# Performance work log

Measured on AMD Instinct MI355X. Metric: run time of the kernel, lower is better.

## Reference

```python
import jax, jax.numpy as jnp
import numpy as np

B, N, D, H = 2, 2048, 512, 8
HD = D // H
EPS = 1e-5


def layernorm(x, g, b):
    m = jnp.mean(x, axis=-1, keepdims=True)
    v = jnp.var(x, axis=-1, keepdims=True)
    return (x - m) * jax.lax.rsqrt(v + EPS) * g + b


def setup_inputs() -> dict:
    key = jax.random.key(0)
    ks = jax.random.split(key, 16)
    s = 1.0 / np.sqrt(D)
    def lin(k, din, dout):
        k1, k2 = jax.random.split(k)
        return (jax.random.uniform(k1, (din, dout), jnp.float32, -s, s),
                jax.random.uniform(k2, (dout,), jnp.float32, -s, s))
    Wq, bq = lin(ks[0], D, D)
    Wk, bk = lin(ks[1], D, D)
    Wv, bv = lin(ks[2], D, D)
    Wo, bo = lin(ks[3], D, D)
    W1, b1 = lin(ks[4], D, 2 * D)
    W2, b2 = lin(ks[5], 2 * D, D)
    return {
        'y': jax.random.normal(ks[6], (B, N, D), jnp.float32),
        'Wq': Wq, 'bq': bq, 'Wk': Wk, 'bk': bk, 'Wv': Wv, 'bv': bv,
        'Wo': Wo, 'bo': bo,
        'ln1_g': jnp.ones((D,)), 'ln1_b': jnp.zeros((D,)),
        'ln2_g': jnp.ones((D,)), 'ln2_b': jnp.zeros((D,)),
        'W1': W1, 'b1': b1, 'W2': W2, 'b2': b2,
    }


def reference(y, Wq, bq, Wk, bk, Wv, bv, Wo, bo, ln1_g, ln1_b, ln2_g, ln2_b, W1, b1, W2, b2):
    x = layernorm(y, ln1_g, ln1_b)
    def heads(W, b):
        return (x @ W + b).reshape(B, N, H, HD).transpose(0, 2, 1, 3)  # bhnc
    q = heads(Wq, bq)
    k = heads(Wk, bk)
    v = heads(Wv, bv)
    score = jax.nn.softmax(jnp.einsum('bhic,bhjc->bhij', q, k) / np.sqrt(HD), axis=-1)
    r = jnp.einsum('bhij,bhjc->bhic', score, v)
    r = r.transpose(0, 2, 1, 3).reshape(B, N, D) @ Wo + bo
    y = y + r
    h = layernorm(y, ln2_g, ln2_b)
    h = jax.nn.gelu(h @ W1 + b1, approximate=False) @ W2 + b2
    return y + h
```

## Files before the change

### kernel.cpp

```cpp
#include <hip/hip_runtime.h>

#define DEVI __device__ __forceinline__

typedef unsigned short u16;
typedef unsigned int   u32;
typedef unsigned long long u64;
typedef float  f32x4  __attribute__((ext_vector_type(4)));
typedef __bf16 bf16x8 __attribute__((ext_vector_type(8)));

union FragU { bf16x8 b; u64 u[2]; __bf16 e[8]; };

DEVI u16 f2b(float x) { __bf16 t = (__bf16)x; return __builtin_bit_cast(u16, t); }

DEVI float exp2a(float x) { float r; asm("v_exp_f32 %0, %1" : "=v"(r) : "v"(x)); return r; }

DEVI void gload16(const void* g, void* l) {
  __builtin_amdgcn_global_load_lds((const __attribute__((address_space(1))) u32*)g,
                                   (__attribute__((address_space(3))) u32*)l, 16, 0, 0);
}

DEVI int swzo(int row, int kb) {
  return ((((kb >> 4) ^ row) & 7) << 4) | ((kb ^ row) & 8) | (kb & 7);
}

DEVI u64 ldswz(const char* base, int row, int kb) {
  return *reinterpret_cast<const u64*>(base + row * 128 + swzo(row, kb));
}

DEVI size_t gaddr(int row, int kbyte, int rowbytes) {
  return (size_t)row * rowbytes + (size_t)((kbyte & ~127) + swzo(row, kbyte & 127));
}

__global__ __launch_bounds__(256)
void transpose_all(const float* __restrict__ Wq, const float* __restrict__ Wk,
                   const float* __restrict__ Wv, const float* __restrict__ Wo,
                   const float* __restrict__ W1, const float* __restrict__ W2,
                   u16* __restrict__ wqkvT, u16* __restrict__ woT,
                   u16* __restrict__ w1T, u16* __restrict__ w2T) {
  __shared__ float tile[32][33];
  const int id = blockIdx.x;
  const float* src; u16* dst; int K, N, bx, by;
  if (id < 1024) {
    const int m = id >> 8, t = id & 255;
    K = 512; N = 512; bx = t & 15; by = t >> 4;
    src = (m == 0) ? Wq : (m == 1) ? Wk : (m == 2) ? Wv : Wo;
    dst = (m == 3) ? woT : wqkvT + m * 512 * 512;
  } else if (id < 1536) {
    const int t = id - 1024; K = 512; N = 1024; bx = t & 31; by = t >> 5;
    src = W1; dst = w1T;
  } else {
    const int t = id - 1536; K = 1024; N = 512; bx = t & 15; by = t >> 4;
    src = W2; dst = w2T;
  }
  const int tx = threadIdx.x & 31, ty = threadIdx.x >> 5;
#pragma unroll
  for (int i = 0; i < 4; ++i)
    tile[ty + i * 8][tx] = src[(size_t)(by * 32 + ty + i * 8) * N + bx * 32 + tx];
  __syncthreads();
#pragma unroll
  for (int i = 0; i < 4; ++i) {
    const int n = bx * 32 + ty + i * 8;
    const int k = by * 32 + tx;
    *(u16*)((char*)dst + gaddr(n, 2 * k, 2 * K)) = f2b(tile[tx][ty + i * 8]);
  }
}

__global__ __launch_bounds__(256)
void ln_bf16(const float* __restrict__ x, const float* __restrict__ g,
             const float* __restrict__ b, char* __restrict__ out) {
  const int row = blockIdx.x;
  const int t = threadIdx.x;
  const float2 v = ((const float2*)(x + (size_t)row * 512))[t];
  float s1 = v.x + v.y, s2 = v.x * v.x + v.y * v.y;
#pragma unroll
  for (int off = 32; off; off >>= 1) { s1 += __shfl_xor(s1, off); s2 += __shfl_xor(s2, off); }
  __shared__ float a1[4], a2[4];
  const int w = t >> 6;
  if ((t & 63) == 0) { a1[w] = s1; a2[w] = s2; }
  __syncthreads();
  s1 = a1[0] + a1[1] + a1[2] + a1[3];
  s2 = a2[0] + a2[1] + a2[2] + a2[3];
  const float mean = s1 * (1.f / 512.f);
  const float var = s2 * (1.f / 512.f) - mean * mean;
  const float rstd = rsqrtf(var + 1e-5f);
  const float2 gg = ((const float2*)g)[t];
  const float2 bb = ((const float2*)b)[t];
  const u16 o0 = f2b((v.x - mean) * rstd * gg.x + bb.x);
  const u16 o1 = f2b((v.y - mean) * rstd * gg.y + bb.y);
  *(u32*)(out + gaddr(row, 4 * t, 1024)) = (u32)o0 | ((u32)o1 << 16);
}

enum { EPI_QKV = 0, EPI_RES = 1, EPI_GELU = 2 };

template <int EPI, int WM, int WN, int AM, int AN>
__global__ __launch_bounds__(WM * WN * 64)
void gemm_bf16(const char* __restrict__ A, const char* __restrict__ Bt, int N, int K,
               const float* __restrict__ bias,
               const float* __restrict__ bq, const float* __restrict__ bk,
               const float* __restrict__ bv,
               const float* __restrict__ res, float* __restrict__ outF,
               char* __restrict__ outB,
               u16* __restrict__ qo, char* __restrict__ ko, char* __restrict__ vo) {
  constexpr int NW = WM * WN;
  constexpr int TM = WM * AM * 16, TN = WN * AN * 16;
  constexpr int NCHA = TM / 8, NCHB = TN / 8, NCH = NCHA + NCHB;
  constexpr int CPW = NCH / NW;
  static_assert(CPW * NW == NCH, "chunk split");
  __shared__ __align__(16) char sA[2][TM * 128];
  __shared__ __align__(16) char sB[2][TN * 128];
  const int tid = threadIdx.x;
  const int l = tid & 63, w = tid >> 6;
  const int tm = blockIdx.x, tn = blockIdx.y;
  const int wr = w / WN, wc = w % WN;
  const int u = l >> 4, r16 = l & 15;
  const int lrow = l >> 3, lgr = l & 7;
  f32x4 acc[AM][AN] = {};
  const size_t KB = (size_t)K * 2;
  const char* Ab = A + (size_t)(tm * TM) * KB;
  const char* Bb = Bt + (size_t)(tn * TN) * KB;
  const int nkt = K >> 6;
  auto stage = [&](int buf, int kt) {
#pragma unroll
    for (int i = 0; i < CPW; ++i) {
      const int c = w * CPW + i;
      if (c < NCHA) {
        gload16(Ab + (size_t)(c * 8 + lrow) * KB + (size_t)kt * 128 + (lgr << 4),
                sA[buf] + c * 1024);
      } else {
        const int c2 = c - NCHA;
        gload16(Bb + (size_t)(c2 * 8 + lrow) * KB + (size_t)kt * 128 + (lgr << 4),
                sB[buf] + c2 * 1024);
      }
    }
  };
  stage(0, 0);
  int cur = 0;
  for (int kt = 0; kt < nkt; ++kt) {
    __syncthreads();
    if (kt + 1 < nkt) stage(cur ^ 1, kt + 1);
    __builtin_amdgcn_s_setprio(1);
#pragma unroll
    for (int ks = 0; ks < 2; ++ks) {
      FragU af[AM], bfr[AN];
      const int kb = ks * 64 + (u << 3);
#pragma unroll
      for (int i = 0; i < AM; ++i) {
        af[i].u[0] = ldswz(sA[cur], wr * (AM * 16) + i * 16 + r16, kb);
        af[i].u[1] = ldswz(sA[cur], wr * (AM * 16) + i * 16 + r16, kb + 32);
      }
#pragma unroll
      for (int i = 0; i < AN; ++i) {
        bfr[i].u[0] = ldswz(sB[cur], wc * (AN * 16) + i * 16 + r16, kb);
        bfr[i].u[1] = ldswz(sB[cur], wc * (AN * 16) + i * 16 + r16, kb + 32);
      }
#pragma unroll
      for (int mi = 0; mi < AM; ++mi)
#pragma unroll
        for (int ni = 0; ni < AN; ++ni)
          acc[mi][ni] = __builtin_amdgcn_mfma_f32_16x16x32_bf16(af[mi].b, bfr[ni].b,
                                                                acc[mi][ni], 0, 0, 0);
    }
    __builtin_amdgcn_s_setprio(0);
    cur ^= 1;
  }
  const int row0 = tm * TM + wr * (AM * 16) + (u << 2);
  const int col0 = tn * TN + wc * (AN * 16) + r16;
#pragma unroll
  for (int mi = 0; mi < AM; ++mi) {
#pragma unroll
    for (int ni = 0; ni < AN; ++ni) {
      const int col = col0 + ni * 16;
      if (EPI == EPI_RES) {
#pragma unroll
        for (int r = 0; r < 4; ++r) {
          const int row = row0 + mi * 16 + r;
          outF[(size_t)row * N + col] = acc[mi][ni][r] + bias[col] + res[(size_t)row * N + col];
        }
      } else if (EPI == EPI_GELU) {
#pragma unroll
        for (int r = 0; r < 4; ++r) {
          const int row = row0 + mi * 16 + r;
          const float x = acc[mi][ni][r] + bias[col];
          *(u16*)(outB + gaddr(row, 2 * col, 2 * N)) =
              f2b(0.5f * x * (1.f + erff(x * 0.70710678118f)));
        }
      } else {
        const int which = col >> 9, cc = col & 511;
        const int h = cc >> 6, hd = cc & 63;
        if (which == 2) {
          const int rowa = row0 + mi * 16;
          const int bb2 = rowa >> 11, nt0 = rowa & 2047;
          const int bh = bb2 * 8 + h;
          const float bvv = bv[cc];
          union { ushort4 s; u64 q; } pk;
          pk.s.x = f2b(acc[mi][ni][0] + bvv);
          pk.s.y = f2b(acc[mi][ni][1] + bvv);
          pk.s.z = f2b(acc[mi][ni][2] + bvv);
          pk.s.w = f2b(acc[mi][ni][3] + bvv);
          *(u64*)(vo + (size_t)bh * 262144 + (size_t)(nt0 >> 6) * 8192 +
                  gaddr(hd, 2 * (nt0 & 63), 128)) = pk.q;
        } else {
#pragma unroll
          for (int r = 0; r < 4; ++r) {
            const int row = row0 + mi * 16 + r;
            const int bb2 = row >> 11, nt = row & 2047;
            const int bh = bb2 * 8 + h;
            if (which == 0)
              qo[((size_t)bh * 2048 + nt) * 64 + hd] = f2b((acc[mi][ni][r] + bq[cc]) * 0.18033688f);
            else
              *(u16*)(ko + (size_t)bh * 262144 + (size_t)(nt >> 6) * 8192 +
                      gaddr(nt & 63, 2 * hd, 128)) = f2b(acc[mi][ni][r] + bk[cc]);
          }
        }
      }
    }
  }
}

__global__ __launch_bounds__(512)
void attn_k(const u16* __restrict__ q, const char* __restrict__ kswz,
            const char* __restrict__ vswz, char* __restrict__ r_out) {
  __shared__ __align__(16) char sK[2][2][8192];
  __shared__ __align__(16) char sV[2][2][8192];
  const int tid = threadIdx.x;
  const int l = tid & 63, w = tid >> 6;
  const int kvh = w & 1, qw = w >> 1;
  const int bh = blockIdx.x, qt = blockIdx.y;
  const int u = l >> 4, r16 = l & 15;
  const char* kp = kswz + (size_t)bh * 262144;
  const char* vp = vswz + (size_t)bh * 262144;
  const int c0 = qw * 2;
  auto stage = [&](int buf, int t) {
#pragma unroll
    for (int c = 0; c < 2; ++c) {
      gload16(kp + (size_t)t * 8192 + (c0 + c) * 1024 + l * 16, sK[kvh][buf] + (c0 + c) * 1024);
      gload16(vp + (size_t)t * 8192 + (c0 + c) * 1024 + l * 16, sV[kvh][buf] + (c0 + c) * 1024);
    }
  };
  stage(0, kvh * 16);
  FragU qf[2];
  {
    const u16* qr = q + (size_t)bh * (2048 * 64) + (size_t)(qt * 64 + qw * 16 + r16) * 64 + (u << 2);
    qf[0].u[0] = *(const u64*)qr;        qf[0].u[1] = *(const u64*)(qr + 16);
    qf[1].u[0] = *(const u64*)(qr + 32); qf[1].u[1] = *(const u64*)(qr + 48);
  }
  float mrun = -1e30f, lrun = 0.f;
  f32x4 o[4] = {};
  int cur = 0;
  for (int i = 0; i < 16; ++i) {
    __syncthreads();
    if (i < 15) stage(cur ^ 1, kvh * 16 + i + 1);
    f32x4 st[4] = {};
    __builtin_amdgcn_s_setprio(1);
#pragma unroll
    for (int ks = 0; ks < 2; ++ks) {
      const int kb = ks * 64 + (u << 3);
#pragma unroll
      for (int mi = 0; mi < 4; ++mi) {
        FragU kf;
        kf.u[0] = ldswz(sK[kvh][cur], mi * 16 + r16, kb);
        kf.u[1] = ldswz(sK[kvh][cur], mi * 16 + r16, kb + 32);
        st[mi] = __builtin_amdgcn_mfma_f32_16x16x32_bf16(kf.b, qf[ks].b, st[mi], 0, 0, 0);
      }
    }
    __builtin_amdgcn_s_setprio(0);
    float tmax = -1e30f;
#pragma unroll
    for (int mi = 0; mi < 4; ++mi)
#pragma unroll
      for (int r = 0; r < 4; ++r) tmax = fmaxf(tmax, st[mi][r]);
    tmax = fmaxf(tmax, __shfl_xor(tmax, 16));
    tmax = fmaxf(tmax, __shfl_xor(tmax, 32));
    if (!__all(tmax <= mrun + 11.5f)) {
      const float mnew = fmaxf(mrun, tmax);
      const float alpha = exp2a(mrun - mnew);
      lrun *= alpha;
#pragma unroll
      for (int mo = 0; mo < 4; ++mo) o[mo] *= alpha;
      mrun = mnew;
    }
    float p[4][4];
    float tsum = 0.f;
#pragma unroll
    for (int mi = 0; mi < 4; ++mi)
#pragma unroll
      for (int r = 0; r < 4; ++r) { p[mi][r] = exp2a(st[mi][r] - mrun); tsum += p[mi][r]; }
    tsum += __shfl_xor(tsum, 16);
    tsum += __shfl_xor(tsum, 32);
    lrun += tsum;
    FragU pb[2];
#pragma unroll
    for (int ks = 0; ks < 2; ++ks)
#pragma unroll
      for (int j = 0; j < 4; ++j) {
        pb[ks].e[j]     = (__bf16)p[2 * ks][j];
        pb[ks].e[j + 4] = (__bf16)p[2 * ks + 1][j];
      }
    __builtin_amdgcn_s_setprio(1);
#pragma unroll
    for (int ks = 0; ks < 2; ++ks) {
      const int kb = ks * 64 + (u << 3);
#pragma unroll
      for (int mo = 0; mo < 4; ++mo) {
        FragU vf;
        vf.u[0] = ldswz(sV[kvh][cur], mo * 16 + r16, kb);
        vf.u[1] = ldswz(sV[kvh][cur], mo * 16 + r16, kb + 32);
        o[mo] = __builtin_amdgcn_mfma_f32_16x16x32_bf16(vf.b, pb[ks].b, o[mo], 0, 0, 0);
      }
    }
    __builtin_amdgcn_s_setprio(0);
    cur ^= 1;
  }
  __syncthreads();
  float* scrO  = (float*)&sK[0][0][0];
  float* scrML = (float*)&sV[0][0][0];
  if (kvh == 1) {
    if (u == 0) { scrML[qw * 32 + r16] = mrun; scrML[qw * 32 + 16 + r16] = lrun; }
#pragma unroll
    for (int mo = 0; mo < 4; ++mo)
#pragma unroll
      for (int r = 0; r < 4; ++r)
        scrO[qw * 1024 + (mo * 16 + u * 4 + r) * 16 + r16] = o[mo][r];
  }
  __syncthreads();
  if (kvh == 0) {
    const float m1 = scrML[qw * 32 + r16], l1 = scrML[qw * 32 + 16 + r16];
    const float m = fmaxf(mrun, m1);
    const float a0 = exp2a(mrun - m), a1 = exp2a(m1 - m);
    const float linv = 1.f / (lrun * a0 + l1 * a1);
    const float f0 = a0 * linv, f1 = a1 * linv;
    const int tok = (bh >> 3) * 2048 + qt * 64 + qw * 16 + r16;
    const int h = bh & 7;
#pragma unroll
    for (int mo = 0; mo < 4; ++mo) {
      union { ushort4 s; u64 qq; } pk;
      float vv[4];
#pragma unroll
      for (int r = 0; r < 4; ++r)
        vv[r] = o[mo][r] * f0 + scrO[qw * 1024 + (mo * 16 + u * 4 + r) * 16 + r16] * f1;
      pk.s.x = f2b(vv[0]); pk.s.y = f2b(vv[1]); pk.s.z = f2b(vv[2]); pk.s.w = f2b(vv[3]);
      *(u64*)(r_out + (size_t)tok * 1024 + h * 128 + swzo(tok, mo * 32 + (u << 3))) = pk.qq;
    }
  }
}

extern "C" void kernel_launch(void* const* d_in, const int* in_sizes, int n_in,
                              void* d_out, int out_size, void* d_ws, size_t ws_size,
                              hipStream_t stream) {
  const float* y    = (const float*)d_in[0];
  const float* Wq   = (const float*)d_in[1];
  const float* bq   = (const float*)d_in[2];
  const float* Wk   = (const float*)d_in[3];
  const float* bk   = (const float*)d_in[4];
  const float* Wv   = (const float*)d_in[5];
  const float* bv   = (const float*)d_in[6];
  const float* Wo   = (const float*)d_in[7];
  const float* bo   = (const float*)d_in[8];
  const float* ln1g = (const float*)d_in[9];
  const float* ln1b = (const float*)d_in[10];
  const float* ln2g = (const float*)d_in[11];
  const float* ln2b = (const float*)d_in[12];
  const float* W1   = (const float*)d_in[13];
  const float* b1   = (const float*)d_in[14];
  const float* W2   = (const float*)d_in[15];
  const float* b2   = (const float*)d_in[16];
  float* out = (float*)d_out;
  char* ws = (char*)d_ws;
  char* xb    = ws;
  u16*  qb    = (u16*)(ws + (4u << 20));
  char* kswz  = ws + (8u << 20);
  char* vswz  = ws + (12u << 20);
  char* rb    = ws + (16u << 20);
  char* g1b   = ws + (20u << 20);
  u16* wqkvT  = (u16*)(ws + (28u << 20));
  u16* woT    = wqkvT + 1536 * 512;
  u16* w1T    = woT + 512 * 512;
  u16* w2T    = w1T + 1024 * 512;

  transpose_all<<<2048, 256, 0, stream>>>(Wq, Wk, Wv, Wo, W1, W2, wqkvT, woT, w1T, w2T);
  ln_bf16<<<4096, 256, 0, stream>>>(y, ln1g, ln1b, xb);
  gemm_bf16<EPI_QKV, 2, 2, 4, 2><<<dim3(32, 24), 256, 0, stream>>>(
      xb, (const char*)wqkvT, 1536, 512, nullptr, bq, bk, bv,
      nullptr, nullptr, nullptr, qb, kswz, vswz);
  attn_k<<<dim3(16, 32), 512, 0, stream>>>(qb, kswz, vswz, rb);
  gemm_bf16<EPI_RES, 2, 2, 2, 2><<<dim3(64, 8), 256, 0, stream>>>(
      rb, (const char*)woT, 512, 512, bo, nullptr, nullptr, nullptr,
      y, out, nullptr, nullptr, nullptr, nullptr);
  ln_bf16<<<4096, 256, 0, stream>>>(out, ln2g, ln2b, xb);
  gemm_bf16<EPI_GELU, 2, 2, 4, 2><<<dim3(32, 16), 256, 0, stream>>>(
      xb, (const char*)w1T, 1024, 512, b1, nullptr, nullptr, nullptr,
      nullptr, nullptr, g1b, nullptr, nullptr, nullptr);
  gemm_bf16<EPI_RES, 2, 2, 2, 2><<<dim3(64, 8), 256, 0, stream>>>(
      g1b, (const char*)w2T, 512, 1024, b2, nullptr, nullptr, nullptr,
      out, out, nullptr, nullptr, nullptr, nullptr);
}
```

Baseline: 104.8 us.

## Fuse weight transpose with first layernorm and fuse Wo GEMM with second layernorm

Merges the weight-transpose kernel and the first layernorm into one launch with branch on block index. Replaces the Wo projection GEMM plus separate layernorm with a new kernel where each 512-thread block computes a full 16-row by 512-column output tile, adds bias and residual, reduces row statistics across waves, and writes both the fp32 residual stream and the bf16 normalized activations. This removes two launches and a round trip of the residual through memory, at the cost of only 256 blocks with B fragments loaded directly from global memory per wave.

```diff
diff --git a/kernel.cpp b/kernel.cpp
--- a/kernel.cpp
+++ b/kernel.cpp
@@ -32,62 +32,62 @@
 }
 
 __global__ __launch_bounds__(256)
-void transpose_all(const float* __restrict__ Wq, const float* __restrict__ Wk,
-                   const float* __restrict__ Wv, const float* __restrict__ Wo,
-                   const float* __restrict__ W1, const float* __restrict__ W2,
-                   u16* __restrict__ wqkvT, u16* __restrict__ woT,
-                   u16* __restrict__ w1T, u16* __restrict__ w2T) {
-  __shared__ float tile[32][33];
+void prep(const float* __restrict__ Wq, const float* __restrict__ Wk,
+          const float* __restrict__ Wv, const float* __restrict__ Wo,
+          const float* __restrict__ W1, const float* __restrict__ W2,
+          u16* __restrict__ wqkvT, u16* __restrict__ woT,
+          u16* __restrict__ w1T, u16* __restrict__ w2T,
+          const float* __restrict__ y, const float* __restrict__ ln1g,
+          const float* __restrict__ ln1b, char* __restrict__ xb) {
   const int id = blockIdx.x;
-  const float* src; u16* dst; int K, N, bx, by;
-  if (id < 1024) {
-    const int m = id >> 8, t = id & 255;
-    K = 512; N = 512; bx = t & 15; by = t >> 4;
-    src = (m == 0) ? Wq : (m == 1) ? Wk : (m == 2) ? Wv : Wo;
-    dst = (m == 3) ? woT : wqkvT + m * 512 * 512;
-  } else if (id < 1536) {
-    const int t = id - 1024; K = 512; N = 1024; bx = t & 31; by = t >> 5;
-    src = W1; dst = w1T;
+  if (id < 2048) {
+    __shared__ float tile[32][33];
+    const float* src; u16* dst; int K, N, bx, by;
+    if (id < 1024) {
+      const int m = id >> 8, t = id & 255;
+      K = 512; N = 512; bx = t & 15; by = t >> 4;
+      src = (m == 0) ? Wq : (m == 1) ? Wk : (m == 2) ? Wv : Wo;
+      dst = (m == 3) ? woT : wqkvT + m * 512 * 512;
+    } else if (id < 1536) {
+      const int t = id - 1024; K = 512; N = 1024; bx = t & 31; by = t >> 5;
+      src = W1; dst = w1T;
+    } else {
+      const int t = id - 1536; K = 1024; N = 512; bx = t & 15; by = t >> 4;
+      src = W2; dst = w2T;
+    }
+    const int tx = threadIdx.x & 31, ty = threadIdx.x >> 5;
+#pragma unroll
+    for (int i = 0; i < 4; ++i)
+      tile[ty + i * 8][tx] = src[(size_t)(by * 32 + ty + i * 8) * N + bx * 32 + tx];
+    __syncthreads();
+#pragma unroll
+    for (int i = 0; i < 4; ++i) {
+      const int n = bx * 32 + ty + i * 8;
+      const int k = by * 32 + tx;
+      *(u16*)((char*)dst + gaddr(n, 2 * k, 2 * K)) = f2b(tile[tx][ty + i * 8]);
+    }
   } else {
-    const int t = id - 1536; K = 1024; N = 512; bx = t & 15; by = t >> 4;
-    src = W2; dst = w2T;
-  }
-  const int tx = threadIdx.x & 31, ty = threadIdx.x >> 5;
-#pragma unroll
-  for (int i = 0; i < 4; ++i)
-    tile[ty + i * 8][tx] = src[(size_t)(by * 32 + ty + i * 8) * N + bx * 32 + tx];
-  __syncthreads();
-#pragma unroll
-  for (int i = 0; i < 4; ++i) {
-    const int n = bx * 32 + ty + i * 8;
-    const int k = by * 32 + tx;
-    *(u16*)((char*)dst + gaddr(n, 2 * k, 2 * K)) = f2b(tile[tx][ty + i * 8]);
-  }
-}
-
-__global__ __launch_bounds__(256)
-void ln_bf16(const float* __restrict__ x, const float* __restrict__ g,
-             const float* __restrict__ b, char* __restrict__ out) {
-  const int row = blockIdx.x;
-  const int t = threadIdx.x;
-  const float2 v = ((const float2*)(x + (size_t)row * 512))[t];
-  float s1 = v.x + v.y, s2 = v.x * v.x + v.y * v.y;
-#pragma unroll
-  for (int off = 32; off; off >>= 1) { s1 += __shfl_xor(s1, off); s2 += __shfl_xor(s2, off); }
-  __shared__ float a1[4], a2[4];
-  const int w = t >> 6;
-  if ((t & 63) == 0) { a1[w] = s1; a2[w] = s2; }
-  __syncthreads();
-  s1 = a1[0] + a1[1] + a1[2] + a1[3];
-  s2 = a2[0] + a2[1] + a2[2] + a2[3];
-  const float mean = s1 * (1.f / 512.f);
-  const float var = s2 * (1.f / 512.f) - mean * mean;
-  const float rstd = rsqrtf(var + 1e-5f);
-  const float2 gg = ((const float2*)g)[t];
-  const float2 bb = ((const float2*)b)[t];
-  const u16 o0 = f2b((v.x - mean) * rstd * gg.x + bb.x);
-  const u16 o1 = f2b((v.y - mean) * rstd * gg.y + bb.y);
-  *(u32*)(out + gaddr(row, 4 * t, 1024)) = (u32)o0 | ((u32)o1 << 16);
+    const int row = id - 2048;
+    const int t = threadIdx.x;
+    const float2 v = ((const float2*)(y + (size_t)row * 512))[t];
+    float s1 = v.x + v.y, s2 = v.x * v.x + v.y * v.y;
+#pragma unroll
+    for (int off = 32; off; off >>= 1) { s1 += __shfl_xor(s1, off); s2 += __shfl_xor(s2, off); }
+    __shared__ float a1[4], a2[4];
+    const int w = t >> 6;
+    if ((t & 63) == 0) { a1[w] = s1; a2[w] = s2; }
+    __syncthreads();
+    s1 = a1[0] + a1[1] + a1[2] + a1[3];
+    s2 = a2[0] + a2[1] + a2[2] + a2[3];
+    const float mean = s1 * (1.f / 512.f);
+    const float var = s2 * (1.f / 512.f) - mean * mean;
+    const float rstd = rsqrtf(var + 1e-5f);
+    const float2 gg = ((const float2*)ln1g)[t];
+    const float2 bb = ((const float2*)ln1b)[t];
+    const u16 o0 = f2b((v.x - mean) * rstd * gg.x + bb.x);
+    const u16 o1 = f2b((v.y - mean) * rstd * gg.y + bb.y);
+    *(u32*)(xb + gaddr(row, 4 * t, 1024)) = (u32)o0 | ((u32)o1 << 16);
+  }
 }
 
 enum { EPI_QKV = 0, EPI_RES = 1, EPI_GELU = 2 };
@@ -213,6 +213,125 @@
           }
         }
       }
+    }
+  }
+}
+
+__global__ __launch_bounds__(512)
+void gemm_res_ln(const char* __restrict__ A, const char* __restrict__ Bt,
+                 const float* __restrict__ bo, const float* __restrict__ yres,
+                 float* __restrict__ outF, const float* __restrict__ g2,
+                 const float* __restrict__ b2v, char* __restrict__ xout) {
+  __shared__ __align__(16) char sA[2][2048];
+  __shared__ float red[2][8][16];
+  __shared__ float stats[2][16];
+  const int tid = threadIdx.x;
+  const int l = tid & 63, w = tid >> 6;
+  const int tm = blockIdx.x;
+  const int u = l >> 4, r16 = l & 15;
+  const int lrow = l >> 3, lgr = l & 7;
+  const char* Ab = A + (size_t)(tm * 16) * 1024;
+  f32x4 acc[4] = {};
+  FragU pa[8], pb[8];
+  auto loadB = [&](FragU* ps, int kt) {
+#pragma unroll
+    for (int ks = 0; ks < 2; ++ks) {
+      const int kb = ks * 64 + (u << 3);
+#pragma unroll
+      for (int ni = 0; ni < 4; ++ni) {
+        const int col = w * 64 + ni * 16 + r16;
+        const char* bp = Bt + (size_t)col * 1024 + kt * 128;
+        ps[ks * 4 + ni].u[0] = *(const u64*)(bp + swzo(col, kb));
+        ps[ks * 4 + ni].u[1] = *(const u64*)(bp + swzo(col, kb + 32));
+      }
+    }
+  };
+  auto stageA = [&](int buf, int kt) {
+    if (w < 2)
+      gload16(Ab + (size_t)(w * 8 + lrow) * 1024 + (size_t)kt * 128 + (lgr << 4),
+              sA[buf] + w * 1024);
+  };
+  auto mmaStep = [&](FragU* ps, int buf) {
+#pragma unroll
+    for (int ks = 0; ks < 2; ++ks) {
+      const int kb = ks * 64 + (u << 3);
+      FragU af;
+      af.u[0] = ldswz(sA[buf], r16, kb);
+      af.u[1] = ldswz(sA[buf], r16, kb + 32);
+#pragma unroll
+      for (int ni = 0; ni < 4; ++ni)
+        acc[ni] = __builtin_amdgcn_mfma_f32_16x16x32_bf16(af.b, ps[ks * 4 + ni].b,
+                                                          acc[ni], 0, 0, 0);
+    }
+  };
+  stageA(0, 0);
+  loadB(pa, 0);
+#pragma unroll
+  for (int kt2 = 0; kt2 < 4; ++kt2) {
+    const int kt = kt2 * 2;
+    __syncthreads();
+    stageA(1, kt + 1);
+    loadB(pb, kt + 1);
+    __builtin_amdgcn_s_setprio(1);
+    mmaStep(pa, 0);
+    __builtin_amdgcn_s_setprio(0);
+    __syncthreads();
+    if (kt + 2 < 8) { stageA(0, kt + 2); loadB(pa, kt + 2); }
+    __builtin_amdgcn_s_setprio(1);
+    mmaStep(pb, 1);
+    __builtin_amdgcn_s_setprio(0);
+  }
+  float x[4][4];
+  float s1r[4] = {}, s2r[4] = {};
+#pragma unroll
+  for (int ni = 0; ni < 4; ++ni) {
+    const int col = w * 64 + ni * 16 + r16;
+#pragma unroll
+    for (int rr = 0; rr < 4; ++rr) {
+      const int row = tm * 16 + u * 4 + rr;
+      const float v = acc[ni][rr] + bo[col] + yres[(size_t)row * 512 + col];
+      x[ni][rr] = v;
+      s1r[rr] += v;
+      s2r[rr] += v * v;
+    }
+  }
+#pragma unroll
+  for (int off = 1; off < 16; off <<= 1) {
+#pragma unroll
+    for (int rr = 0; rr < 4; ++rr) {
+      s1r[rr] += __shfl_xor(s1r[rr], off);
+      s2r[rr] += __shfl_xor(s2r[rr], off);
+    }
+  }
+  if (r16 == 0) {
+#pragma unroll
+    for (int rr = 0; rr < 4; ++rr) {
+      red[0][w][u * 4 + rr] = s1r[rr];
+      red[1][w][u * 4 + rr] = s2r[rr];
+    }
+  }
+  __syncthreads();
+  if (tid < 16) {
+    float s1 = 0.f, s2 = 0.f;
+#pragma unroll
+    for (int ww = 0; ww < 8; ++ww) { s1 += red[0][ww][tid]; s2 += red[1][ww][tid]; }
+    const float mean = s1 * (1.f / 512.f);
+    const float var = s2 * (1.f / 512.f) - mean * mean;
+    stats[0][tid] = mean;
+    stats[1][tid] = rsqrtf(var + 1e-5f);
+  }
+  __syncthreads();
+#pragma unroll
+  for (int ni = 0; ni < 4; ++ni) {
+    const int col = w * 64 + ni * 16 + r16;
+    const float gg = g2[col], bb = b2v[col];
+#pragma unroll
+    for (int rr = 0; rr < 4; ++rr) {
+      const int rl = u * 4 + rr;
+      const int row = tm * 16 + rl;
+      outF[(size_t)row * 512 + col] = x[ni][rr];
+      const float ln = (x[ni][rr] - stats[0][rl]) * stats[1][rl] * gg + bb;
+      *(u16*)(xout + gaddr(row, 2 * col, 1024)) = f2b(ln);
     }
   }
 }
@@ -377,16 +496,14 @@
   u16* w1T    = woT + 512 * 512;
   u16* w2T    = w1T + 1024 * 512;
 
-  transpose_all<<<2048, 256, 0, stream>>>(Wq, Wk, Wv, Wo, W1, W2, wqkvT, woT, w1T, w2T);
-  ln_bf16<<<4096, 256, 0, stream>>>(y, ln1g, ln1b, xb);
+  prep<<<6144, 256, 0, stream>>>(Wq, Wk, Wv, Wo, W1, W2, wqkvT, woT, w1T, w2T,
+                                 y, ln1g, ln1b, xb);
   gemm_bf16<EPI_QKV, 2, 2, 4, 2><<<dim3(32, 24), 256, 0, stream>>>(
       xb, (const char*)wqkvT, 1536, 512, nullptr, bq, bk, bv,
       nullptr, nullptr, nullptr, qb, kswz, vswz);
   attn_k<<<dim3(16, 32), 512, 0, stream>>>(qb, kswz, vswz, rb);
-  gemm_bf16<EPI_RES, 2, 2, 2, 2><<<dim3(64, 8), 256, 0, stream>>>(
-      rb, (const char*)woT, 512, 512, bo, nullptr, nullptr, nullptr,
-      y, out, nullptr, nullptr, nullptr, nullptr);
-  ln_bf16<<<4096, 256, 0, stream>>>(out, ln2g, ln2b, xb);
+  gemm_res_ln<<<256, 512, 0, stream>>>(
+      rb, (const char*)woT, bo, y, out, ln2g, ln2b, xb);
   gemm_bf16<EPI_GELU, 2, 2, 4, 2><<<dim3(32, 16), 256, 0, stream>>>(
       xb, (const char*)w1T, 1024, 512, b1, nullptr, nullptr, nullptr,
       nullptr, nullptr, g1b, nullptr, nullptr, nullptr);
```

Result: no change. 106.4 us (+1.5%).

## Merge weight transpose with first layernorm; restructure attention K/V staging

Applied to the files above, without the earlier changes.

The weight transpose and the first layernorm now run as a single launch, which removes one kernel launch and its tail. The transpose also writes packed 8-byte stores instead of 2-byte scalar stores. The attention kernel now processes two KV tiles per iteration, with K and V loaded into both buffers and restaged separately. The next K block loads while softmax and PV run, and the next V block loads after PV. This halves the loop trips and barriers but raises register pressure (8 score accumulators) and drops the old double-buffered overlap of QK with loads.

```diff
diff --git a/kernel.cpp b/kernel.cpp
--- a/kernel.cpp
+++ b/kernel.cpp
@@ -32,36 +32,64 @@
 }
 
 __global__ __launch_bounds__(256)
-void transpose_all(const float* __restrict__ Wq, const float* __restrict__ Wk,
-                   const float* __restrict__ Wv, const float* __restrict__ Wo,
-                   const float* __restrict__ W1, const float* __restrict__ W2,
-                   u16* __restrict__ wqkvT, u16* __restrict__ woT,
-                   u16* __restrict__ w1T, u16* __restrict__ w2T) {
-  __shared__ float tile[32][33];
+void prep(const float* __restrict__ Wq, const float* __restrict__ Wk,
+          const float* __restrict__ Wv, const float* __restrict__ Wo,
+          const float* __restrict__ W1, const float* __restrict__ W2,
+          u16* __restrict__ wqkvT, u16* __restrict__ woT,
+          u16* __restrict__ w1T, u16* __restrict__ w2T,
+          const float* __restrict__ y, const float* __restrict__ ln1g,
+          const float* __restrict__ ln1b, char* __restrict__ xb) {
   const int id = blockIdx.x;
-  const float* src; u16* dst; int K, N, bx, by;
-  if (id < 1024) {
-    const int m = id >> 8, t = id & 255;
-    K = 512; N = 512; bx = t & 15; by = t >> 4;
-    src = (m == 0) ? Wq : (m == 1) ? Wk : (m == 2) ? Wv : Wo;
-    dst = (m == 3) ? woT : wqkvT + m * 512 * 512;
-  } else if (id < 1536) {
-    const int t = id - 1024; K = 512; N = 1024; bx = t & 31; by = t >> 5;
-    src = W1; dst = w1T;
+  if (id < 2048) {
+    __shared__ float tile[32][33];
+    const float* src; u16* dst; int K, N, bx, by;
+    if (id < 1024) {
+      const int m = id >> 8, t = id & 255;
+      K = 512; N = 512; bx = t & 15; by = t >> 4;
+      src = (m == 0) ? Wq : (m == 1) ? Wk : (m == 2) ? Wv : Wo;
+      dst = (m == 3) ? woT : wqkvT + m * 512 * 512;
+    } else if (id < 1536) {
+      const int t = id - 1024; K = 512; N = 1024; bx = t & 31; by = t >> 5;
+      src = W1; dst = w1T;
+    } else {
+      const int t = id - 1536; K = 1024; N = 512; bx = t & 15; by = t >> 4;
+      src = W2; dst = w2T;
+    }
+    const int tx = threadIdx.x & 31, ty = threadIdx.x >> 5;
+#pragma unroll
+    for (int i = 0; i < 4; ++i)
+      tile[ty + i * 8][tx] = src[(size_t)(by * 32 + ty + i * 8) * N + bx * 32 + tx];
+    __syncthreads();
+    const int nl = threadIdx.x >> 3, kq = threadIdx.x & 7;
+    const int n = bx * 32 + nl;
+    const int kg = by * 32 + kq * 4;
+    union { ushort4 s; u64 q; } pk;
+    pk.s.x = f2b(tile[kq * 4 + 0][nl]);
+    pk.s.y = f2b(tile[kq * 4 + 1][nl]);
+    pk.s.z = f2b(tile[kq * 4 + 2][nl]);
+    pk.s.w = f2b(tile[kq * 4 + 3][nl]);
+    *(u64*)((char*)dst + gaddr(n, 2 * kg, 2 * K)) = pk.q;
   } else {
-    const int t = id - 1536; K = 1024; N = 512; bx = t & 15; by = t >> 4;
-    src = W2; dst = w2T;
-  }
-  const int tx = threadIdx.x & 31, ty = threadIdx.x >> 5;
-#pragma unroll
-  for (int i = 0; i < 4; ++i)
-    tile[ty + i * 8][tx] = src[(size_t)(by * 32 + ty + i * 8) * N + bx * 32 + tx];
-  __syncthreads();
-#pragma unroll
-  for (int i = 0; i < 4; ++i) {
-    const int n = bx * 32 + ty + i * 8;
-    const int k = by * 32 + tx;
-    *(u16*)((char*)dst + gaddr(n, 2 * k, 2 * K)) = f2b(tile[tx][ty + i * 8]);
+    const int row = id - 2048;
+    const int t = threadIdx.x;
+    const float2 v = ((const float2*)(y + (size_t)row * 512))[t];
+    float s1 = v.x + v.y, s2 = v.x * v.x + v.y * v.y;
+#pragma unroll
+    for (int off = 32; off; off >>= 1) { s1 += __shfl_xor(s1, off); s2 += __shfl_xor(s2, off); }
+    __shared__ float a1[4], a2[4];
+    const int w = t >> 6;
+    if ((t & 63) == 0) { a1[w] = s1; a2[w] = s2; }
+    __syncthreads();
+    s1 = a1[0] + a1[1] + a1[2] + a1[3];
+    s2 = a2[0] + a2[1] + a2[2] + a2[3];
+    const float mean = s1 * (1.f / 512.f);
+    const float var = s2 * (1.f / 512.f) - mean * mean;
+    const float rstd = rsqrtf(var + 1e-5f);
+    const float2 gg = ((const float2*)ln1g)[t];
+    const float2 bb = ((const float2*)ln1b)[t];
+    const u16 o0 = f2b((v.x - mean) * rstd * gg.x + bb.x);
+    const u16 o1 = f2b((v.y - mean) * rstd * gg.y + bb.y);
+    *(u32*)(xb + gaddr(row, 4 * t, 1024)) = (u32)o0 | ((u32)o1 << 16);
   }
 }
 
@@ -230,14 +258,24 @@
   const char* kp = kswz + (size_t)bh * 262144;
   const char* vp = vswz + (size_t)bh * 262144;
   const int c0 = qw * 2;
-  auto stage = [&](int buf, int t) {
+  auto stageK = [&](int j) {
+    const size_t t0 = (size_t)(kvh * 16 + 2 * j) * 8192;
 #pragma unroll
     for (int c = 0; c < 2; ++c) {
-      gload16(kp + (size_t)t * 8192 + (c0 + c) * 1024 + l * 16, sK[kvh][buf] + (c0 + c) * 1024);
-      gload16(vp + (size_t)t * 8192 + (c0 + c) * 1024 + l * 16, sV[kvh][buf] + (c0 + c) * 1024);
+      gload16(kp + t0 + (c0 + c) * 1024 + l * 16, sK[kvh][0] + (c0 + c) * 1024);
+      gload16(kp + t0 + 8192 + (c0 + c) * 1024 + l * 16, sK[kvh][1] + (c0 + c) * 1024);
     }
   };
-  stage(0, kvh * 16);
+  auto stageV = [&](int j) {
+    const size_t t0 = (size_t)(kvh * 16 + 2 * j) * 8192;
+#pragma unroll
+    for (int c = 0; c < 2; ++c) {
+      gload16(vp + t0 + (c0 + c) * 1024 + l * 16, sV[kvh][0] + (c0 + c) * 1024);
+      gload16(vp + t0 + 8192 + (c0 + c) * 1024 + l * 16, sV[kvh][1] + (c0 + c) * 1024);
+    }
+  };
+  stageK(0);
+  stageV(0);
   FragU qf[2];
   {
     const u16* qr = q + (size_t)bh * (2048 * 64) + (size_t)(qt * 64 + qw * 16 + r16) * 64 + (u << 2);
@@ -246,29 +284,32 @@
   }
   float mrun = -1e30f, lrun = 0.f;
   f32x4 o[4] = {};
-  int cur = 0;
-  for (int i = 0; i < 16; ++i) {
+  __syncthreads();
+  for (int j = 0; j < 8; ++j) {
+    f32x4 st[8] = {};
+    __builtin_amdgcn_s_setprio(1);
+#pragma unroll
+    for (int buf = 0; buf < 2; ++buf)
+#pragma unroll
+      for (int ks = 0; ks < 2; ++ks) {
+        const int kb = ks * 64 + (u << 3);
+#pragma unroll
+        for (int mi = 0; mi < 4; ++mi) {
+          FragU kf;
+          kf.u[0] = ldswz(sK[kvh][buf], mi * 16 + r16, kb);
+          kf.u[1] = ldswz(sK[kvh][buf], mi * 16 + r16, kb + 32);
+          st[buf * 4 + mi] = __builtin_amdgcn_mfma_f32_16x16x32_bf16(kf.b, qf[ks].b,
+                                                                     st[buf * 4 + mi], 0, 0, 0);
+        }
+      }
+    __builtin_amdgcn_s_setprio(0);
     __syncthreads();
-    if (i < 15) stage(cur ^ 1, kvh * 16 + i + 1);
-    f32x4 st[4] = {};
-    __builtin_amdgcn_s_setprio(1);
-#pragma unroll
-    for (int ks = 0; ks < 2; ++ks) {
-      const int kb = ks * 64 + (u << 3);
-#pragma unroll
-      for (int mi = 0; mi < 4; ++mi) {
-        FragU kf;
-        kf.u[0] = ldswz(sK[kvh][cur], mi * 16 + r16, kb);
-        kf.u[1] = ldswz(sK[kvh][cur], mi * 16 + r16, kb + 32);
-        st[mi] = __builtin_amdgcn_mfma_f32_16x16x32_bf16(kf.b, qf[ks].b, st[mi], 0, 0, 0);
-      }
-    }
-    __builtin_amdgcn_s_setprio(0);
+    if (j < 7) stageK(j + 1);
     float tmax = -1e30f;
 #pragma unroll
-    for (int mi = 0; mi < 4; ++mi)
-#pragma unroll
-      for (int r = 0; r < 4; ++r) tmax = fmaxf(tmax, st[mi][r]);
+    for (int i = 0; i < 8; ++i)
+#pragma unroll
+      for (int r = 0; r < 4; ++r) tmax = fmaxf(tmax, st[i][r]);
     tmax = fmaxf(tmax, __shfl_xor(tmax, 16));
     tmax = fmaxf(tmax, __shfl_xor(tmax, 32));
     if (!__all(tmax <= mrun + 11.5f)) {
@@ -279,37 +320,42 @@
       for (int mo = 0; mo < 4; ++mo) o[mo] *= alpha;
       mrun = mnew;
     }
-    float p[4][4];
     float tsum = 0.f;
 #pragma unroll
-    for (int mi = 0; mi < 4; ++mi)
-#pragma unroll
-      for (int r = 0; r < 4; ++r) { p[mi][r] = exp2a(st[mi][r] - mrun); tsum += p[mi][r]; }
+    for (int i = 0; i < 8; ++i)
+#pragma unroll
+      for (int r = 0; r < 4; ++r) { st[i][r] = exp2a(st[i][r] - mrun); tsum += st[i][r]; }
     tsum += __shfl_xor(tsum, 16);
     tsum += __shfl_xor(tsum, 32);
     lrun += tsum;
-    FragU pb[2];
-#pragma unroll
-    for (int ks = 0; ks < 2; ++ks)
-#pragma unroll
-      for (int j = 0; j < 4; ++j) {
-        pb[ks].e[j]     = (__bf16)p[2 * ks][j];
-        pb[ks].e[j + 4] = (__bf16)p[2 * ks + 1][j];
-      }
+    FragU pb[4];
+#pragma unroll
+    for (int buf = 0; buf < 2; ++buf)
+#pragma unroll
+      for (int ks = 0; ks < 2; ++ks)
+#pragma unroll
+        for (int jj = 0; jj < 4; ++jj) {
+          pb[buf * 2 + ks].e[jj]     = (__bf16)st[buf * 4 + 2 * ks][jj];
+          pb[buf * 2 + ks].e[jj + 4] = (__bf16)st[buf * 4 + 2 * ks + 1][jj];
+        }
     __builtin_amdgcn_s_setprio(1);
 #pragma unroll
-    for (int ks = 0; ks < 2; ++ks) {
-      const int kb = ks * 64 + (u << 3);
-#pragma unroll
-      for (int mo = 0; mo < 4; ++mo) {
-        FragU vf;
-        vf.u[0] = ldswz(sV[kvh][cur], mo * 16 + r16, kb);
-        vf.u[1] = ldswz(sV[kvh][cur], mo * 16 + r16, kb + 32);
-        o[mo] = __builtin_amdgcn_mfma_f32_16x16x32_bf16(vf.b, pb[ks].b, o[mo], 0, 0, 0);
-      }
-    }
+    for (int buf = 0; buf < 2; ++buf)
+#pragma unroll
+      for (int ks = 0; ks < 2; ++ks) {
+        const int kb = ks * 64 + (u << 3);
+#pragma unroll
+        for (int mo = 0; mo < 4; ++mo) {
+          FragU vf;
+          vf.u[0] = ldswz(sV[kvh][buf], mo * 16 + r16, kb);
+          vf.u[1] = ldswz(sV[kvh][buf], mo * 16 + r16, kb + 32);
+          o[mo] = __builtin_amdgcn_mfma_f32_16x16x32_bf16(vf.b, pb[buf * 2 + ks].b,
+                                                          o[mo], 0, 0, 0);
+        }
+      }
     __builtin_amdgcn_s_setprio(0);
-    cur ^= 1;
+    __syncthreads();
+    if (j < 7) stageV(j + 1);
   }
   __syncthreads();
   float* scrO  = (float*)&sK[0][0][0];
@@ -377,8 +423,8 @@
   u16* w1T    = woT + 512 * 512;
   u16* w2T    = w1T + 1024 * 512;
 
-  transpose_all<<<2048, 256, 0, stream>>>(Wq, Wk, Wv, Wo, W1, W2, wqkvT, woT, w1T, w2T);
-  ln_bf16<<<4096, 256, 0, stream>>>(y, ln1g, ln1b, xb);
+  prep<<<6144, 256, 0, stream>>>(Wq, Wk, Wv, Wo, W1, W2, wqkvT, woT, w1T, w2T,
+                                 y, ln1g, ln1b, xb);
   gemm_bf16<EPI_QKV, 2, 2, 4, 2><<<dim3(32, 24), 256, 0, stream>>>(
       xb, (const char*)wqkvT, 1536, 512, nullptr, bq, bk, bv,
       nullptr, nullptr, nullptr, qb, kswz, vswz);
```

Measured after the change: 110.9 us. +5.8%, slower.
